# Kernel tuning notes

Hardware: AMD Instinct MI355X
Metric: run time of the kernel (lower is better)

## Reference

```python
import jax, jax.numpy as jnp
import numpy as np

N = 50000   # nodes
E = 150000  # edges
G = 256     # graphs in batch
H0, H1, H2, H3 = 8, 128, 256, 512


def _lin(key, fi, fo):
    return jax.random.normal(key, (fi, fo), dtype=jnp.float32) * (1.0 / np.sqrt(fi))


def setup_inputs() -> dict:
    key = jax.random.key(0)
    ks = jax.random.split(key, 12)
    x = jax.random.normal(ks[0], (N, H0), dtype=jnp.float32)
    edge_index = jax.random.randint(ks[1], (2, E), 0, N)
    edge_weight = jax.random.uniform(ks[2], (E,), dtype=jnp.float32)
    batch = jnp.sort(jax.random.randint(ks[3], (N,), 0, G))
    return {
        'x': x, 'edge_index': edge_index, 'edge_weight': edge_weight, 'batch': batch,
        'W1': _lin(ks[4], H0, H1), 'b1': jnp.zeros((H1,), jnp.float32),
        'W2': _lin(ks[5], H1, H2), 'b2': jnp.zeros((H2,), jnp.float32),
        'W3': _lin(ks[6], H2, H3), 'b3': jnp.zeros((H3,), jnp.float32),
        'Wfc': _lin(ks[7], H3, 1), 'bfc': jnp.zeros((1,), jnp.float32),
    }


def _gcn_conv(h, W, b, src, dst, ew, n):
    # h: [N, Fin] -> [N, Fout]; symmetric GCN normalization (self-loops already in src/dst/ew)
    h = h @ W                                             # [N, Fout]
    deg = jax.ops.segment_sum(ew, dst, num_segments=n)    # [N]
    dinv = jnp.where(deg > 0, jax.lax.rsqrt(deg), 0.0)
    norm = dinv[src] * ew * dinv[dst]                     # [E+N]
    msgs = h[src] * norm[:, None]                         # gather + scale
    out = jax.ops.segment_sum(msgs, dst, num_segments=n)  # scatter-add
    return out + b


def reference(x, edge_index, edge_weight, batch, W1, b1, W2, b2, W3, b3, Wfc, bfc):
    n = x.shape[0]
    loop = jnp.arange(n)
    src = jnp.concatenate([edge_index[0], loop])
    dst = jnp.concatenate([edge_index[1], loop])
    ew = jnp.concatenate([edge_weight, jnp.ones((n,), edge_weight.dtype)])

    h1 = jax.nn.relu(_gcn_conv(x, W1, b1, src, dst, ew, n))
    h2 = jax.nn.relu(_gcn_conv(h1, W2, b2, src, dst, ew, n))
    h3 = jax.nn.relu(_gcn_conv(h2, W3, b3, src, dst, ew, n))

    # global mean pool over graphs
    sums = jax.ops.segment_sum(h3, batch, num_segments=G)              # [G, H3]
    cnt = jax.ops.segment_sum(jnp.ones((n,), h3.dtype), batch, num_segments=G)
    pooled = sums / jnp.maximum(cnt, 1.0)[:, None]

    return jax.nn.sigmoid(pooled @ Wfc + bfc)              # [G, 1]
```

## Files before the change

### kernel.cpp

```cpp
#include <hip/hip_runtime.h>
#include <math.h>

typedef __attribute__((ext_vector_type(8))) short short8;
typedef __attribute__((ext_vector_type(4))) float floatx4;


__device__ __forceinline__ unsigned short f2bf(float f) {
    unsigned int u = __float_as_uint(f);
    unsigned int r = (u + 0x7fffu + ((u >> 16) & 1u)) >> 16;
    return (unsigned short)r;
}
__device__ __forceinline__ float bfu_lo(unsigned int u) {
    return __uint_as_float(u << 16);
}
__device__ __forceinline__ float bfu_hi(unsigned int u) {
    return __uint_as_float(u & 0xffff0000u);
}


__global__ void k_init_wt(float* __restrict__ deg, int* __restrict__ cnt,
                          int* __restrict__ cursor, int N,
                          const float* __restrict__ W2, unsigned short* __restrict__ WT2,
                          int K2, int F2,
                          const float* __restrict__ W3, unsigned short* __restrict__ WT3,
                          int K3, int F3) {
    int i = blockIdx.x * blockDim.x + threadIdx.x;
    if (i < N) { deg[i] = 1.0f; cnt[i] = 0; cursor[i] = 0; }
    int n2 = K2 * F2;
    if (i < n2) {
        int k = i / F2, n = i % F2;
        WT2[(size_t)n * K2 + k] = f2bf(W2[i]);
    } else {
        int j = i - n2;
        if (j < K3 * F3) {
            int k = j / F3, n = j % F3;
            WT3[(size_t)n * K3 + k] = f2bf(W3[j]);
        }
    }
}

__global__ void k_hist_deg(const int* __restrict__ dst, const float* __restrict__ ew,
                           float* __restrict__ deg, int* __restrict__ cnt, int E) {
    int e = blockIdx.x * blockDim.x + threadIdx.x;
    if (e < E) {
        int d = dst[e];
        atomicAdd(&deg[d], ew[e]);
        atomicAdd(&cnt[d], 1);
    }
}

__global__ __launch_bounds__(256) void k_dinv_scana(float* __restrict__ deg,
                                                    const int* __restrict__ cnt,
                                                    int* __restrict__ bsum, int N) {
    int b = blockIdx.x, t = threadIdx.x;
    int base = b * 1024 + t * 4;
    int s = 0;
#pragma unroll
    for (int j = 0; j < 4; ++j) {
        int i = base + j;
        if (i < N) { deg[i] = rsqrtf(deg[i]); s += cnt[i]; }
    }
    __shared__ int sh[256];
    sh[t] = s; __syncthreads();
    for (int st = 128; st > 0; st >>= 1) { if (t < st) sh[t] += sh[t + st]; __syncthreads(); }
    if (t == 0) bsum[b] = sh[0];
}

__global__ __launch_bounds__(256) void k_scan_c(const int* __restrict__ cnt,
                                                const int* __restrict__ bsum,
                                                int* __restrict__ row_start, int N, int nb) {
    int b = blockIdx.x, t = threadIdx.x;
    __shared__ int sh[256];
    __shared__ int boffs;

    if (t < 64) {
        int s = 0;
        for (int i = t; i < b; i += 64) s += bsum[i];
#pragma unroll
        for (int off = 32; off > 0; off >>= 1) s += __shfl_down(s, off);
        if (t == 0) boffs = s;
    }
    __syncthreads();

    int base = b * 1024 + t * 4;
    int v[4]; int s = 0;
#pragma unroll
    for (int j = 0; j < 4; ++j) { int i = base + j; v[j] = (i < N) ? cnt[i] : 0; s += v[j]; }
    sh[t] = s; __syncthreads();
    for (int off = 1; off < 256; off <<= 1) {
        int x = (t >= off) ? sh[t - off] : 0;
        __syncthreads();
        sh[t] += x;
        __syncthreads();
    }
    int excl = sh[t] - s + boffs;
#pragma unroll
    for (int j = 0; j < 4; ++j) {
        int i = base + j;
        if (i < N) row_start[i] = excl;
        excl += v[j];
        if (i == N - 1) row_start[N] = excl;
    }
}

__global__ void k_scatter_norm(const int* __restrict__ src, const int* __restrict__ dst,
                               const float* __restrict__ ew, const float* __restrict__ dinv,
                               const int* __restrict__ row_start, int* __restrict__ cursor,
                               int* __restrict__ esrc, float* __restrict__ enorm, int E) {
    int e = blockIdx.x * blockDim.x + threadIdx.x;
    if (e >= E) return;
    int d = dst[e], s = src[e];
    int pos = row_start[d] + atomicAdd(&cursor[d], 1);
    esrc[pos] = s;
    enorm[pos] = dinv[s] * ew[e] * dinv[d];
}


__global__ __launch_bounds__(256) void k_l1_gemm(
    const float* __restrict__ x, const float* __restrict__ dinv,
    const int* __restrict__ esrc, const float* __restrict__ enorm,
    const int* __restrict__ row_start, const float* __restrict__ W1,
    const float* __restrict__ b1, unsigned short* __restrict__ h1, int N) {
    __shared__ float As[8][132];
    __shared__ float Bs[8][128];

    int tid = threadIdx.x;
    int bm = blockIdx.x * 128;

#pragma unroll
    for (int i = tid; i < 1024; i += 256) Bs[i >> 7][i & 127] = W1[i];

    if (tid < 128) {
        int n = bm + tid;
        float a[8] = {0, 0, 0, 0, 0, 0, 0, 0};
        if (n < N) {
            float dv = dinv[n];
            float dv2 = dv * dv;
            float4 v0 = *(const float4*)&x[(size_t)n * 8];
            float4 v1 = *(const float4*)&x[(size_t)n * 8 + 4];
            a[0] = v0.x * dv2; a[1] = v0.y * dv2; a[2] = v0.z * dv2; a[3] = v0.w * dv2;
            a[4] = v1.x * dv2; a[5] = v1.y * dv2; a[6] = v1.z * dv2; a[7] = v1.w * dv2;
            int j0 = row_start[n], j1 = row_start[n + 1];
            for (int b = j0; b < j1; b += 4) {
                int i1 = (b + 1 < j1) ? b + 1 : b;
                int i2 = (b + 2 < j1) ? b + 2 : b;
                int i3 = (b + 3 < j1) ? b + 3 : b;
                float w0 = enorm[b];
                float w1 = (b + 1 < j1) ? enorm[i1] : 0.f;
                float w2 = (b + 2 < j1) ? enorm[i2] : 0.f;
                float w3 = (b + 3 < j1) ? enorm[i3] : 0.f;
                int s0 = esrc[b], s1 = esrc[i1], s2 = esrc[i2], s3 = esrc[i3];
                float4 p0 = *(const float4*)&x[(size_t)s0 * 8];
                float4 q0 = *(const float4*)&x[(size_t)s0 * 8 + 4];
                float4 p1 = *(const float4*)&x[(size_t)s1 * 8];
                float4 q1 = *(const float4*)&x[(size_t)s1 * 8 + 4];
                float4 p2 = *(const float4*)&x[(size_t)s2 * 8];
                float4 q2 = *(const float4*)&x[(size_t)s2 * 8 + 4];
                float4 p3 = *(const float4*)&x[(size_t)s3 * 8];
                float4 q3 = *(const float4*)&x[(size_t)s3 * 8 + 4];
                a[0] += w0 * p0.x + w1 * p1.x + w2 * p2.x + w3 * p3.x;
                a[1] += w0 * p0.y + w1 * p1.y + w2 * p2.y + w3 * p3.y;
                a[2] += w0 * p0.z + w1 * p1.z + w2 * p2.z + w3 * p3.z;
                a[3] += w0 * p0.w + w1 * p1.w + w2 * p2.w + w3 * p3.w;
                a[4] += w0 * q0.x + w1 * q1.x + w2 * q2.x + w3 * q3.x;
                a[5] += w0 * q0.y + w1 * q1.y + w2 * q2.y + w3 * q3.y;
                a[6] += w0 * q0.z + w1 * q1.z + w2 * q2.z + w3 * q3.z;
                a[7] += w0 * q0.w + w1 * q1.w + w2 * q2.w + w3 * q3.w;
            }
        }
#pragma unroll
        for (int k = 0; k < 8; ++k) As[k][tid] = a[k];
    }
    __syncthreads();

    int tx = tid & 15;
    int ty = tid >> 4;
    float acc[8][8];
#pragma unroll
    for (int i = 0; i < 8; ++i)
#pragma unroll
        for (int j = 0; j < 8; ++j) acc[i][j] = 0.f;

#pragma unroll
    for (int k = 0; k < 8; ++k) {
        float a[8], b[8];
        float4 a0 = *(const float4*)&As[k][ty * 4];
        float4 a1 = *(const float4*)&As[k][ty * 4 + 64];
        float4 b0 = *(const float4*)&Bs[k][tx * 4];
        float4 b1 = *(const float4*)&Bs[k][tx * 4 + 64];
        a[0] = a0.x; a[1] = a0.y; a[2] = a0.z; a[3] = a0.w;
        a[4] = a1.x; a[5] = a1.y; a[6] = a1.z; a[7] = a1.w;
        b[0] = b0.x; b[1] = b0.y; b[2] = b0.z; b[3] = b0.w;
        b[4] = b1.x; b[5] = b1.y; b[6] = b1.z; b[7] = b1.w;
#pragma unroll
        for (int i = 0; i < 8; ++i)
#pragma unroll
            for (int j = 0; j < 8; ++j) acc[i][j] += a[i] * b[j];
    }

    float4 bi0 = *(const float4*)&b1[tx * 4];
    float4 bi1 = *(const float4*)&b1[tx * 4 + 64];
    float bb[8] = {bi0.x, bi0.y, bi0.z, bi0.w, bi1.x, bi1.y, bi1.z, bi1.w};
#pragma unroll
    for (int i = 0; i < 8; ++i) {
        int gm = bm + ((i < 4) ? (ty * 4 + i) : (64 + ty * 4 + i - 4));
        if (gm >= N) continue;
        ushort4 v0, v1;
        v0.x = f2bf(fmaxf(acc[i][0] + bb[0], 0.f));
        v0.y = f2bf(fmaxf(acc[i][1] + bb[1], 0.f));
        v0.z = f2bf(fmaxf(acc[i][2] + bb[2], 0.f));
        v0.w = f2bf(fmaxf(acc[i][3] + bb[3], 0.f));
        v1.x = f2bf(fmaxf(acc[i][4] + bb[4], 0.f));
        v1.y = f2bf(fmaxf(acc[i][5] + bb[5], 0.f));
        v1.z = f2bf(fmaxf(acc[i][6] + bb[6], 0.f));
        v1.w = f2bf(fmaxf(acc[i][7] + bb[7], 0.f));
        *(ushort4*)&h1[(size_t)gm * 128 + tx * 4] = v0;
        *(ushort4*)&h1[(size_t)gm * 128 + tx * 4 + 64] = v1;
    }
}


__global__ void k_agg_bf(const unsigned short* __restrict__ h, const float* __restrict__ dinv,
                         const int* __restrict__ esrc, const float* __restrict__ enorm,
                         const int* __restrict__ row_start,
                         unsigned short* __restrict__ A,
                         int N, int Mpad, int F, int osh) {
    int p = blockIdx.x * blockDim.x + threadIdx.x;
    int oct = F >> 3;
    if (p >= Mpad * oct) return;
    int n = p >> osh;
    int fo = (p & (oct - 1)) << 3;
    size_t oidx = (size_t)n * F + fo;
    if (n >= N) {
        *(uint4*)&A[oidx] = make_uint4(0, 0, 0, 0);
        return;
    }
    float dv = dinv[n];
    float dv2 = dv * dv;
    uint4 hv = *(const uint4*)&h[oidx];
    float s0 = bfu_lo(hv.x) * dv2, s1 = bfu_hi(hv.x) * dv2;
    float s2 = bfu_lo(hv.y) * dv2, s3 = bfu_hi(hv.y) * dv2;
    float s4 = bfu_lo(hv.z) * dv2, s5 = bfu_hi(hv.z) * dv2;
    float s6 = bfu_lo(hv.w) * dv2, s7 = bfu_hi(hv.w) * dv2;
    int j0 = row_start[n], j1 = row_start[n + 1];
    for (int b = j0; b < j1; b += 4) {
        int i1 = (b + 1 < j1) ? b + 1 : b;
        int i2 = (b + 2 < j1) ? b + 2 : b;
        int i3 = (b + 3 < j1) ? b + 3 : b;
        float w0 = enorm[b];
        float w1 = (b + 1 < j1) ? enorm[i1] : 0.f;
        float w2 = (b + 2 < j1) ? enorm[i2] : 0.f;
        float w3 = (b + 3 < j1) ? enorm[i3] : 0.f;
        int e0 = esrc[b], e1 = esrc[i1], e2 = esrc[i2], e3 = esrc[i3];
        uint4 r0 = *(const uint4*)&h[(size_t)e0 * F + fo];
        uint4 r1 = *(const uint4*)&h[(size_t)e1 * F + fo];
        uint4 r2 = *(const uint4*)&h[(size_t)e2 * F + fo];
        uint4 r3 = *(const uint4*)&h[(size_t)e3 * F + fo];
        s0 += w0 * bfu_lo(r0.x) + w1 * bfu_lo(r1.x) + w2 * bfu_lo(r2.x) + w3 * bfu_lo(r3.x);
        s1 += w0 * bfu_hi(r0.x) + w1 * bfu_hi(r1.x) + w2 * bfu_hi(r2.x) + w3 * bfu_hi(r3.x);
        s2 += w0 * bfu_lo(r0.y) + w1 * bfu_lo(r1.y) + w2 * bfu_lo(r2.y) + w3 * bfu_lo(r3.y);
        s3 += w0 * bfu_hi(r0.y) + w1 * bfu_hi(r1.y) + w2 * bfu_hi(r2.y) + w3 * bfu_hi(r3.y);
        s4 += w0 * bfu_lo(r0.z) + w1 * bfu_lo(r1.z) + w2 * bfu_lo(r2.z) + w3 * bfu_lo(r3.z);
        s5 += w0 * bfu_hi(r0.z) + w1 * bfu_hi(r1.z) + w2 * bfu_hi(r2.z) + w3 * bfu_hi(r3.z);
        s6 += w0 * bfu_lo(r0.w) + w1 * bfu_lo(r1.w) + w2 * bfu_lo(r2.w) + w3 * bfu_lo(r3.w);
        s7 += w0 * bfu_hi(r0.w) + w1 * bfu_hi(r1.w) + w2 * bfu_hi(r2.w) + w3 * bfu_hi(r3.w);
    }
    uint4 o;
    o.x = (unsigned int)f2bf(s0) | ((unsigned int)f2bf(s1) << 16);
    o.y = (unsigned int)f2bf(s2) | ((unsigned int)f2bf(s3) << 16);
    o.z = (unsigned int)f2bf(s4) | ((unsigned int)f2bf(s5) << 16);
    o.w = (unsigned int)f2bf(s6) | ((unsigned int)f2bf(s7) << 16);
    *(uint4*)&A[oidx] = o;
}


template <int EPI>
__global__ __launch_bounds__(256, 4) void k_gemm_async(
    const unsigned short* __restrict__ A, const unsigned short* __restrict__ B,
    const float* __restrict__ bias, unsigned short* __restrict__ C,
    const float* __restrict__ Wfc, float* __restrict__ part,
    int M, int Mpad, int K, int Fout, int nbsh) {
    __shared__ __align__(16) unsigned short smem[8192];

    int tid = threadIdx.x, wave = tid >> 6, lane = tid & 63;
    int quad = lane >> 4, r = lane & 15;

    int P = blockIdx.x;
    int r8 = P & 7;
    int q = P >> 3;
    int bnIdx = q & ((1 << nbsh) - 1);
    int g = ((q >> nbsh) << 3) + r8;
    int bm = g * 128, bn = bnIdx * 128;
    int wm = (wave & 1) * 64, wn = (wave >> 1) * 64;

    const unsigned short* gsrc[2] = {A, B};
    const int rb[2] = {bm, bn};

    floatx4 acc[4][4] = {};

    for (int k0 = 0; k0 < K; k0 += 32) {
#pragma unroll
        for (int t = 0; t < 2; ++t) {
#pragma unroll
            for (int i = 0; i < 2; ++i) {
                int qc = wave * 2 + i;
                int idx = qc * 64 + lane;
                int row = idx >> 2, kofs = (idx & 3) << 3;
                const unsigned short* gptr = gsrc[t] + ((size_t)(rb[t] + row) * K + k0 + kofs);
                unsigned short* l = &smem[t * 4096 + qc * 512];
                __builtin_amdgcn_global_load_lds(
                    (const __attribute__((address_space(1))) void*)gptr,
                    (__attribute__((address_space(3))) void*)l, 16, 0, 0);
            }
        }
        __syncthreads();

        short8 ah[4];
#pragma unroll
        for (int mt = 0; mt < 4; ++mt) {
            int m = wm + mt * 16 + r;
            ah[mt] = *(const short8*)&smem[m * 32 + quad * 8];
        }
#pragma unroll
        for (int nt = 0; nt < 4; ++nt) {
            int n = wn + nt * 16 + r;
            short8 bh = *(const short8*)&smem[4096 + n * 32 + quad * 8];
#pragma unroll
            for (int mt = 0; mt < 4; ++mt)
                acc[mt][nt] = __builtin_amdgcn_mfma_f32_16x16x32_bf16(ah[mt], bh, acc[mt][nt], 0, 0, 0);
        }
        __syncthreads();
    }

    float bv[4];
#pragma unroll
    for (int nt = 0; nt < 4; ++nt) bv[nt] = bias[bn + wn + nt * 16 + r];

    if (EPI == 0) {
        float* eps = (float*)&smem[0] + wave * 1024;
#pragma unroll
        for (int mt = 0; mt < 4; ++mt) {
#pragma unroll
            for (int nt = 0; nt < 4; ++nt)
#pragma unroll
                for (int reg = 0; reg < 4; ++reg)
                    eps[(quad * 4 + reg) * 64 + nt * 16 + r] =
                        fmaxf(acc[mt][nt][reg] + bv[nt], 0.f);
#pragma unroll
            for (int i = 0; i < 4; ++i) {
                int fl = i * 64 + lane;
                int ri = fl >> 4, c4 = fl & 15;
                float4 v = *(const float4*)&eps[ri * 64 + c4 * 4];
                int gm = bm + wm + mt * 16 + ri;
                if (gm < M)
                    *(ushort4*)&C[(size_t)gm * Fout + bn + wn + c4 * 4] =
                        make_ushort4(f2bf(v.x), f2bf(v.y), f2bf(v.z), f2bf(v.w));
            }
        }
    } else {
        float* rowsum = (float*)&smem[0];
        if (tid < 128) rowsum[tid] = 0.f;
        __syncthreads();
        float wf[4];
#pragma unroll
        for (int nt = 0; nt < 4; ++nt) wf[nt] = Wfc[bn + wn + nt * 16 + r];
#pragma unroll
        for (int mt = 0; mt < 4; ++mt)
#pragma unroll
            for (int reg = 0; reg < 4; ++reg) {
                float v = 0.f;
#pragma unroll
                for (int nt = 0; nt < 4; ++nt)
                    v += fmaxf(acc[mt][nt][reg] + bv[nt], 0.f) * wf[nt];
                v += __shfl_xor(v, 1);
                v += __shfl_xor(v, 2);
                v += __shfl_xor(v, 4);
                v += __shfl_xor(v, 8);
                if (r == 0) atomicAdd(&rowsum[wm + mt * 16 + quad * 4 + reg], v);
            }
        __syncthreads();
        if (tid < 128) part[(size_t)bnIdx * Mpad + bm + tid] = rowsum[tid];
    }
}


__global__ __launch_bounds__(256) void k_pool2(const float* __restrict__ part,
                                               const int* __restrict__ batch,
                                               const float* __restrict__ bfc,
                                               float* __restrict__ out,
                                               int N, int Mpad, int nchunks, int G) {
    int g = (int)((blockIdx.x * blockDim.x + threadIdx.x) >> 6);
    int lane = threadIdx.x & 63;
    if (g >= G) return;
    int lo = 0, hi = N;
    while (lo < hi) { int m = (lo + hi) >> 1; if (batch[m] < g) lo = m + 1; else hi = m; }
    int start = lo;
    hi = N;
    while (lo < hi) { int m = (lo + hi) >> 1; if (batch[m] < g + 1) lo = m + 1; else hi = m; }
    int end = lo;
    float s = 0.f;
    for (int i = start + lane; i < end; i += 64) {
        float t = 0.f;
        for (int c = 0; c < nchunks; ++c) t += part[(size_t)c * Mpad + i];
        s += t;
    }
#pragma unroll
    for (int off = 32; off > 0; off >>= 1) s += __shfl_down(s, off);
    if (lane == 0) {
        float c = (float)(end - start);
        if (c < 1.f) c = 1.f;
        float z = s / c + bfc[0];
        out[g] = 1.f / (1.f + expf(-z));
    }
}


static inline int cdiv(int a, int b) { return (a + b - 1) / b; }

extern "C" void kernel_launch(void* const* d_in, const int* in_sizes, int n_in,
                              void* d_out, int out_size, void* d_ws, size_t ws_size,
                              hipStream_t stream) {
    const float* x   = (const float*)d_in[0];
    const int*   ei  = (const int*)d_in[1];
    const float* ew  = (const float*)d_in[2];
    const int*   bat = (const int*)d_in[3];
    const float* W1  = (const float*)d_in[4];
    const float* b1  = (const float*)d_in[5];
    const float* W2  = (const float*)d_in[6];
    const float* b2  = (const float*)d_in[7];
    const float* W3  = (const float*)d_in[8];
    const float* b3  = (const float*)d_in[9];
    const float* Wfc = (const float*)d_in[10];
    const float* bfc = (const float*)d_in[11];
    float* out = (float*)d_out;

    const int N  = in_sizes[3];
    const int E  = in_sizes[2];
    const int H1 = in_sizes[5];
    const int H2 = in_sizes[7];
    const int H3 = in_sizes[9];
    const int G  = out_size;
    const int Mpad = cdiv(N, 1024) * 1024;
    const int Npad4 = (N + 4) & ~3;

    const int* srcv = ei;
    const int* dstv = ei + E;

    char* p = (char*)d_ws;
    float* dinv      = (float*)p; p += (size_t)N * 4;
    int*   cnt       = (int*)p;   p += (size_t)N * 4;
    int*   cursor    = (int*)p;   p += (size_t)N * 4;
    int*   bsum      = (int*)p;   p += 256 * 4;
    int*   row_start = (int*)p;   p += (size_t)Npad4 * 4;
    int*   esrc      = (int*)p;   p += (size_t)E * 4;
    float* enorm     = (float*)p; p += (size_t)E * 4;
    float* part      = (float*)p; p += (size_t)(H3 / 128) * Mpad * 4;
    unsigned short* WT2 = (unsigned short*)p; p += (size_t)H1 * H2 * 2;
    unsigned short* WT3 = (unsigned short*)p; p += (size_t)H2 * H3 * 2;
    unsigned short* Abf = (unsigned short*)p; p += (size_t)Mpad * H2 * 2;
    unsigned short* h1  = (unsigned short*)p; p += (size_t)Mpad * H1 * 2;
    unsigned short* h2  = (unsigned short*)p; p += (size_t)Mpad * H2 * 2;

    int initTot = H1 * H2 + H2 * H3;
    if (initTot < N) initTot = N;
    k_init_wt<<<cdiv(initTot, 256), 256, 0, stream>>>(dinv, cnt, cursor, N,
                                                      W2, WT2, H1, H2, W3, WT3, H2, H3);
    k_hist_deg<<<cdiv(E, 256), 256, 0, stream>>>(dstv, ew, dinv, cnt, E);
    int nb = cdiv(N, 1024);
    k_dinv_scana<<<nb, 256, 0, stream>>>(dinv, cnt, bsum, N);
    k_scan_c<<<nb, 256, 0, stream>>>(cnt, bsum, row_start, N, nb);
    k_scatter_norm<<<cdiv(E, 256), 256, 0, stream>>>(srcv, dstv, ew, dinv, row_start,
                                                     cursor, esrc, enorm, E);

    k_l1_gemm<<<cdiv(N, 128), 256, 0, stream>>>(x, dinv, esrc, enorm, row_start, W1, b1, h1, N);

    k_agg_bf<<<cdiv(Mpad * (H1 / 8), 256), 256, 0, stream>>>(
        h1, dinv, esrc, enorm, row_start, Abf, N, Mpad, H1, __builtin_ctz(H1) - 3);
    k_gemm_async<0><<<(Mpad / 128) * (H2 / 128), 256, 0, stream>>>(
        Abf, WT2, b2, h2, nullptr, nullptr, N, Mpad, H1, H2, __builtin_ctz(H2 / 128));

    k_agg_bf<<<cdiv(Mpad * (H2 / 8), 256), 256, 0, stream>>>(
        h2, dinv, esrc, enorm, row_start, Abf, N, Mpad, H2, __builtin_ctz(H2) - 3);
    k_gemm_async<1><<<(Mpad / 128) * (H3 / 128), 256, 0, stream>>>(
        Abf, WT3, b3, nullptr, Wfc, part, N, Mpad, H2, H3, __builtin_ctz(H3 / 128));

    k_pool2<<<cdiv(G * 64, 256), 256, 0, stream>>>(part, bat, bfc, out, N, Mpad, H3 / 128, G);
}
```

Measured before the change: 217.9 us.

## Double GEMM K-step to 64 and split layer-1 aggregation across two threads per node

The bf16 MFMA GEMM now stages two 32-wide K slices per iteration into twice the shared memory. This halves the number of barrier pairs per tile and issues more async global-to-LDS loads in flight. Separately, the layer-1 neighbor aggregation now uses all 256 threads, with two threads per node each handling four features, instead of only 128 threads. The cost is more LDS per block (32KB), which may limit occupancy under the 4-blocks launch bound, plus duplicated edge index and weight loads per node.

After: 212.3 us. 2.6% less time.

```diff
diff --git a/kernel.cpp b/kernel.cpp
--- a/kernel.cpp
+++ b/kernel.cpp
@@ -130,16 +130,16 @@
 #pragma unroll
     for (int i = tid; i < 1024; i += 256) Bs[i >> 7][i & 127] = W1[i];
 
-    if (tid < 128) {
-        int n = bm + tid;
-        float a[8] = {0, 0, 0, 0, 0, 0, 0, 0};
+    {
+        int node = tid >> 1;
+        int half = tid & 1;
+        int n = bm + node;
+        float a[4] = {0, 0, 0, 0};
         if (n < N) {
             float dv = dinv[n];
             float dv2 = dv * dv;
-            float4 v0 = *(const float4*)&x[(size_t)n * 8];
-            float4 v1 = *(const float4*)&x[(size_t)n * 8 + 4];
+            float4 v0 = *(const float4*)&x[(size_t)n * 8 + half * 4];
             a[0] = v0.x * dv2; a[1] = v0.y * dv2; a[2] = v0.z * dv2; a[3] = v0.w * dv2;
-            a[4] = v1.x * dv2; a[5] = v1.y * dv2; a[6] = v1.z * dv2; a[7] = v1.w * dv2;
             int j0 = row_start[n], j1 = row_start[n + 1];
             for (int b = j0; b < j1; b += 4) {
                 int i1 = (b + 1 < j1) ? b + 1 : b;
@@ -150,26 +150,18 @@
                 float w2 = (b + 2 < j1) ? enorm[i2] : 0.f;
                 float w3 = (b + 3 < j1) ? enorm[i3] : 0.f;
                 int s0 = esrc[b], s1 = esrc[i1], s2 = esrc[i2], s3 = esrc[i3];
-                float4 p0 = *(const float4*)&x[(size_t)s0 * 8];
-                float4 q0 = *(const float4*)&x[(size_t)s0 * 8 + 4];
-                float4 p1 = *(const float4*)&x[(size_t)s1 * 8];
-                float4 q1 = *(const float4*)&x[(size_t)s1 * 8 + 4];
-                float4 p2 = *(const float4*)&x[(size_t)s2 * 8];
-                float4 q2 = *(const float4*)&x[(size_t)s2 * 8 + 4];
-                float4 p3 = *(const float4*)&x[(size_t)s3 * 8];
-                float4 q3 = *(const float4*)&x[(size_t)s3 * 8 + 4];
+                float4 p0 = *(const float4*)&x[(size_t)s0 * 8 + half * 4];
+                float4 p1 = *(const float4*)&x[(size_t)s1 * 8 + half * 4];
+                float4 p2 = *(const float4*)&x[(size_t)s2 * 8 + half * 4];
+                float4 p3 = *(const float4*)&x[(size_t)s3 * 8 + half * 4];
                 a[0] += w0 * p0.x + w1 * p1.x + w2 * p2.x + w3 * p3.x;
                 a[1] += w0 * p0.y + w1 * p1.y + w2 * p2.y + w3 * p3.y;
                 a[2] += w0 * p0.z + w1 * p1.z + w2 * p2.z + w3 * p3.z;
                 a[3] += w0 * p0.w + w1 * p1.w + w2 * p2.w + w3 * p3.w;
-                a[4] += w0 * q0.x + w1 * q1.x + w2 * q2.x + w3 * q3.x;
-                a[5] += w0 * q0.y + w1 * q1.y + w2 * q2.y + w3 * q3.y;
-                a[6] += w0 * q0.z + w1 * q1.z + w2 * q2.z + w3 * q3.z;
-                a[7] += w0 * q0.w + w1 * q1.w + w2 * q2.w + w3 * q3.w;
             }
         }
 #pragma unroll
-        for (int k = 0; k < 8; ++k) As[k][tid] = a[k];
+        for (int k = 0; k < 4; ++k) As[half * 4 + k][node] = a[k];
     }
     __syncthreads();
 
@@ -280,7 +272,7 @@
     const float* __restrict__ bias, unsigned short* __restrict__ C,
     const float* __restrict__ Wfc, float* __restrict__ part,
     int M, int Mpad, int K, int Fout, int nbsh) {
-    __shared__ __align__(16) unsigned short smem[8192];
+    __shared__ __align__(16) unsigned short smem[16384];
 
     int tid = threadIdx.x, wave = tid >> 6, lane = tid & 63;
     int quad = lane >> 4, r = lane & 15;
@@ -298,36 +290,44 @@
 
     floatx4 acc[4][4] = {};
 
-    for (int k0 = 0; k0 < K; k0 += 32) {
+    for (int k0 = 0; k0 < K; k0 += 64) {
 #pragma unroll
         for (int t = 0; t < 2; ++t) {
 #pragma unroll
-            for (int i = 0; i < 2; ++i) {
-                int qc = wave * 2 + i;
-                int idx = qc * 64 + lane;
-                int row = idx >> 2, kofs = (idx & 3) << 3;
-                const unsigned short* gptr = gsrc[t] + ((size_t)(rb[t] + row) * K + k0 + kofs);
-                unsigned short* l = &smem[t * 4096 + qc * 512];
-                __builtin_amdgcn_global_load_lds(
-                    (const __attribute__((address_space(1))) void*)gptr,
-                    (__attribute__((address_space(3))) void*)l, 16, 0, 0);
+            for (int w = 0; w < 2; ++w) {
+#pragma unroll
+                for (int i = 0; i < 2; ++i) {
+                    int qc = wave * 2 + i;
+                    int idx = qc * 64 + lane;
+                    int row = idx >> 2, kofs = (idx & 3) << 3;
+                    const unsigned short* gptr =
+                        gsrc[t] + ((size_t)(rb[t] + row) * K + k0 + w * 32 + kofs);
+                    unsigned short* l = &smem[(t * 2 + w) * 4096 + qc * 512];
+                    __builtin_amdgcn_global_load_lds(
+                        (const __attribute__((address_space(1))) void*)gptr,
+                        (__attribute__((address_space(3))) void*)l, 16, 0, 0);
+                }
             }
         }
         __syncthreads();
 
-        short8 ah[4];
-#pragma unroll
-        for (int mt = 0; mt < 4; ++mt) {
-            int m = wm + mt * 16 + r;
-            ah[mt] = *(const short8*)&smem[m * 32 + quad * 8];
-        }
-#pragma unroll
-        for (int nt = 0; nt < 4; ++nt) {
-            int n = wn + nt * 16 + r;
-            short8 bh = *(const short8*)&smem[4096 + n * 32 + quad * 8];
-#pragma unroll
-            for (int mt = 0; mt < 4; ++mt)
-                acc[mt][nt] = __builtin_amdgcn_mfma_f32_16x16x32_bf16(ah[mt], bh, acc[mt][nt], 0, 0, 0);
+#pragma unroll
+        for (int w = 0; w < 2; ++w) {
+            short8 ah[4];
+#pragma unroll
+            for (int mt = 0; mt < 4; ++mt) {
+                int m = wm + mt * 16 + r;
+                ah[mt] = *(const short8*)&smem[w * 4096 + m * 32 + quad * 8];
+            }
+#pragma unroll
+            for (int nt = 0; nt < 4; ++nt) {
+                int n = wn + nt * 16 + r;
+                short8 bh = *(const short8*)&smem[(2 + w) * 4096 + n * 32 + quad * 8];
+#pragma unroll
+                for (int mt = 0; mt < 4; ++mt)
+                    acc[mt][nt] =
+                        __builtin_amdgcn_mfma_f32_16x16x32_bf16(ah[mt], bh, acc[mt][nt], 0, 0, 0);
+            }
         }
         __syncthreads();
     }
```
